# Kernel tuning notes

Hardware: AMD Instinct MI355X
Metric: run time of the kernel (lower is better)

Reference implementation:

```python
import jax, jax.numpy as jnp
import numpy as np

K = 3            # pairwise_size
DIL = 2          # pairwise_dilation
COLOR_THRESH = 0.3
EOS_COEF = 0.1


def unfold_wo_center(x, k, d):
    """x: [N,1,H,W] -> [N,1,k*k-1,H,W]; zero-padded dilated neighborhood, center removed
    (equivalent to F.unfold(x, k, padding=(k//2)*d, dilation=d) minus center tap)."""
    N, C, H, W = x.shape
    pad = (k // 2) * d
    xp = jnp.pad(x, ((0, 0), (0, 0), (pad, pad), (pad, pad)))
    c = k // 2
    patches = []
    for i in range(k):
        for j in range(k):
            if i == c and j == c:
                continue
            patches.append(xp[:, :, i * d:i * d + H, j * d:j * d + W])
    return jnp.stack(patches, axis=2)


def setup_inputs() -> dict:
    key = jax.random.key(0)
    k1, k2, k3, k4, k5 = jax.random.split(key, 5)
    B, Q, C1 = 2, 100, 81          # batch, queries, num_classes+1
    N, H, W = 64, 256, 256         # matched instances, mask resolution
    pred_logits = jax.random.normal(k1, (B, Q, C1), jnp.float32)
    target_classes = jax.random.randint(k2, (B, Q), 0, C1)
    src_masks = jax.random.normal(k3, (N, H, W), jnp.float32)
    target_box_masks = jax.random.randint(k4, (N, H, W), 0, 2).astype(jnp.int32)
    target_similarities = jax.random.uniform(k5, (N, K * K - 1, H, W), jnp.float32)
    empty_weight = jnp.ones((C1,), jnp.float32).at[-1].set(EOS_COEF)
    return {
        "pred_logits": pred_logits,
        "src_masks": src_masks,
        "empty_weight": empty_weight,
        "target_similarities": target_similarities,
        "target_classes": target_classes,
        "target_box_masks": target_box_masks,
        "num_masks": 64,
    }


def reference(pred_logits, src_masks, empty_weight, target_similarities,
              target_classes, target_box_masks, num_masks):
    nm = jnp.float32(max(int(num_masks), 1))

    # ---- loss_labels: weighted cross entropy (PyTorch weighted mean) ----
    logp = jax.nn.log_softmax(pred_logits.astype(jnp.float32), axis=-1)
    nll = -jnp.take_along_axis(logp, target_classes[..., None], axis=-1)[..., 0]
    w = empty_weight[target_classes]
    loss_ce = (w * nll).sum() / w.sum()

    # ---- loss_pairwise: BoxInst-style log-prob affinity over dilated neighborhood ----
    x = src_masks[:, None]                      # [N,1,H,W]
    lfg = jax.nn.log_sigmoid(x)
    lbg = jax.nn.log_sigmoid(-x)
    fg_u = unfold_wo_center(lfg, K, DIL)        # [N,1,8,H,W]
    bg_u = unfold_wo_center(lbg, K, DIL)
    a = lfg[:, :, None] + fg_u                  # log P(both fg)
    b = lbg[:, :, None] + bg_u                  # log P(both bg)
    m = jnp.maximum(a, b)
    log_same = jnp.log(jnp.exp(a - m) + jnp.exp(b - m)) + m
    sim = -log_same[:, 0]                       # [N,8,H,W]
    tgt = (target_similarities >= COLOR_THRESH).astype(jnp.float32) \
          * target_box_masks[:, None].astype(jnp.float32)
    loss_pairwise = (sim * tgt).sum() / jnp.maximum(tgt.sum(), 1.0) / nm
    # warmup_factor = 1.0 (iter >= pairwise_warmup_iters)

    # ---- loss_projection_masks: 1D projection dice ----
    eps = 0.001
    tb = target_box_masks.astype(jnp.float32)
    ix = jax.nn.sigmoid(src_masks.max(axis=2))  # project over W -> [N,H]
    iy = jax.nn.sigmoid(src_masks.max(axis=1))  # project over H -> [N,W]
    tx = tb.max(axis=2)
    ty = tb.max(axis=1)
    lx = 1.0 - 2.0 * (ix * tx).sum(1) / ((ix ** 2).sum(1) + (tx ** 2).sum(1) + eps)
    ly = 1.0 - 2.0 * (iy * ty).sum(1) / ((iy ** 2).sum(1) + (ty ** 2).sum(1) + eps)
    loss_proj = (lx + ly).sum() / nm

    return loss_ce + loss_pairwise + loss_proj
```

## Files before the change

kernel.cpp:

```cpp
#include <hip/hip_runtime.h>
#include <hip/hip_bf16.h>
#include <cmath>

#define H 256
#define W 256
#define NIMG 64
#define HW 65536
#define NBLK 2048
#define NWAVE (NBLK * 4)

typedef float vf4 __attribute__((ext_vector_type(4)));

__device__ inline float waveReduceSum(float v) {
#pragma unroll
    for (int o = 32; o > 0; o >>= 1) v += __shfl_xor(v, o, 64);
    return v;
}
__device__ inline float waveReduceMax(float v) {
#pragma unroll
    for (int o = 32; o > 0; o >>= 1) v = fmaxf(v, __shfl_xor(v, o, 64));
    return v;
}
__device__ inline float blockReduceSum(float v, float* s) {
    int lane = threadIdx.x & 63, wv = threadIdx.x >> 6;
    v = waveReduceSum(v);
    if (lane == 0) s[wv] = v;
    __syncthreads();
    float r = 0.f;
    if (wv == 0) {
        r = (lane < 4) ? s[lane] : 0.f;
        r = waveReduceSum(r);
    }
    __syncthreads();
    return r;
}

__global__ __launch_bounds__(256) void k_prep(
    const float* __restrict__ src, const int* __restrict__ bm,
    float* __restrict__ sigma,
    float* __restrict__ colpart_x, float* __restrict__ colpart_b,
    float* __restrict__ rowmax_x, float* __restrict__ rowmax_b)
{
    __shared__ float sx[32][4];
    __shared__ float sb[32][4];
    const int chunk = blockIdx.x, n = blockIdx.y, t = threadIdx.x;
    const int lane = t & 63, wv = t >> 6;
    const size_t base = (size_t)n * HW + chunk * 32 * W + t;
    const float* s = src + base;
    const int* b = bm + base;
    float* sg = sigma + base;
    float mx = -3.4e38f, mb = 0.f;
#pragma unroll 4
    for (int r = 0; r < 32; r++) {
        const float x = s[r * W];
        const float bf = (float)b[r * W];
        sg[r * W] = __builtin_amdgcn_rcpf(1.f + __expf(-x));
        mx = fmaxf(mx, x);
        mb = fmaxf(mb, bf);
        const float rx = waveReduceMax(x);
        const float rb = waveReduceMax(bf);
        if (lane == 0) { sx[r][wv] = rx; sb[r][wv] = rb; }
    }
    const int o = (n * 8 + chunk) * W + t;
    colpart_x[o] = mx;
    colpart_b[o] = mb;
    __syncthreads();
    if (t < 32) {
        rowmax_x[n * H + chunk * 32 + t] =
            fmaxf(fmaxf(sx[t][0], sx[t][1]), fmaxf(sx[t][2], sx[t][3]));
    } else if (t < 64) {
        const int r = t - 32;
        rowmax_b[n * H + chunk * 32 + r] =
            fmaxf(fmaxf(sb[r][0], sb[r][1]), fmaxf(sb[r][2], sb[r][3]));
    }
}

__global__ __launch_bounds__(256, 4) void k_stream(
    const float* __restrict__ ts, const int* __restrict__ bm,
    const float* __restrict__ sigma,
    float* __restrict__ part_st, float* __restrict__ part_t)
{
    const int t = threadIdx.x, lane = t & 63, wv = t >> 6;
    const int wid = blockIdx.x * 4 + wv;
    const int c0 = lane << 2;
    const int lm = (lane + 63) & 63, lp = (lane + 1) & 63;

    const int h  = wid & 255;
    const int p  = (wid >> 8) & 7;
    const int n0 = wid >> 11;

    const int DR = (p < 3) ? -2 : ((p < 5) ? 0 : 2);
    const int DC = (p == 0 || p == 3 || p == 5) ? -2 : ((p == 1 || p == 6) ? 0 : 2);
    const int hn = h + DR;
    const bool rv = (hn >= 0) && (hn < H);
    const int hnc = rv ? hn : h;

    const float* tsp0 = ts + ((size_t)(n0 * 8 + p)) * HW + (size_t)h * W + c0;
    const int*   bmp0 = bm + (size_t)n0 * HW + (size_t)h * W + c0;
    const float* scp0 = sigma + (size_t)n0 * HW + (size_t)h * W + c0;
    const float* snp0 = sigma + (size_t)n0 * HW + (size_t)hnc * W + c0;
    const size_t tstride = (size_t)4 * 8 * HW;
    const size_t istride = (size_t)4 * HW;

    float st = 0.f, tt = 0.f;

    vf4 Ats = __builtin_nontemporal_load(reinterpret_cast<const vf4*>(tsp0));
    int4   Abm = *reinterpret_cast<const int4*>(bmp0);
    float4 Asc = *reinterpret_cast<const float4*>(scp0);
    float4 Asn = *reinterpret_cast<const float4*>(snp0);

#pragma unroll 1
    for (int k = 0; k < 16; k++) {
        vf4 Bts = Ats; int4 Bbm = Abm; float4 Bsc = Asc; float4 Bsn = Asn;
        if (k < 15) {
            Bts = __builtin_nontemporal_load(
                reinterpret_cast<const vf4*>(tsp0 + (size_t)(k + 1) * tstride));
            Bbm = *reinterpret_cast<const int4*>(bmp0 + (size_t)(k + 1) * istride);
            Bsc = *reinterpret_cast<const float4*>(scp0 + (size_t)(k + 1) * istride);
            Bsn = *reinterpret_cast<const float4*>(snp0 + (size_t)(k + 1) * istride);
        }
        const float win[8] = {
            __shfl(Asn.z, lm, 64), __shfl(Asn.w, lm, 64),
            Asn.x, Asn.y, Asn.z, Asn.w,
            __shfl(Asn.x, lp, 64), __shfl(Asn.y, lp, 64)
        };
        const float scv[4] = {Asc.x, Asc.y, Asc.z, Asc.w};
        const float tsv[4] = {Ats.x, Ats.y, Ats.z, Ats.w};
        const int   bmv[4] = {Abm.x, Abm.y, Abm.z, Abm.w};
        float prod = 1.f;
#pragma unroll
        for (int i = 0; i < 4; i++) {
            const float sc = scv[i];
            const float bmf = (float)bmv[i];
            const bool thr = (tsv[i] >= 0.3f);
            tt += thr ? bmf : 0.f;
            const int col = c0 + i + DC;
            const bool valid = rv && (col >= 0) && (col < W);
            const float sn = (DC == -2) ? win[i] : ((DC == 0) ? win[i + 2] : win[i + 4]);
            const float P = fmaf(2.f * sc, sn, (1.f - sc) - sn);
            prod *= (thr && valid && (bmv[i] != 0)) ? P : 1.f;
        }
        st -= __logf(prod);
        Ats = Bts; Abm = Bbm; Asc = Bsc; Asn = Bsn;
    }
    const float wst = waveReduceSum(st);
    const float wtt = waveReduceSum(tt);
    if (lane == 0) { part_st[wid] = wst; part_t[wid] = wtt; }
}

__global__ __launch_bounds__(256) void k_proj(
    const float* __restrict__ colpart_x, const float* __restrict__ colpart_b,
    const float* __restrict__ rowmax_x, const float* __restrict__ rowmax_b,
    float* __restrict__ proj)
{
    __shared__ float red[4];
    const int n = blockIdx.x, t = threadIdx.x;
    float cx = -3.4e38f, cb = 0.f;
#pragma unroll
    for (int c = 0; c < 8; c++) {
        cx = fmaxf(cx, colpart_x[(n * 8 + c) * W + t]);
        cb = fmaxf(cb, colpart_b[(n * 8 + c) * W + t]);
    }
    const float iy = 1.f / (1.f + expf(-cx));
    const float ty = cb;
    const float ix = 1.f / (1.f + expf(-rowmax_x[n * H + t]));
    const float tx = rowmax_b[n * H + t];

    const float Sxy = blockReduceSum(ix * tx, red);
    const float Sxx = blockReduceSum(ix * ix, red);
    const float Stx = blockReduceSum(tx * tx, red);
    const float Syw = blockReduceSum(iy * ty, red);
    const float Syy = blockReduceSum(iy * iy, red);
    const float Sty = blockReduceSum(ty * ty, red);
    if (t == 0) {
        const float eps = 0.001f;
        const float lx = 1.f - 2.f * Sxy / (Sxx + Stx + eps);
        const float ly = 1.f - 2.f * Syw / (Syy + Sty + eps);
        proj[n] = lx + ly;
    }
}

__global__ __launch_bounds__(256) void k_final(
    const float* __restrict__ logits, const int* __restrict__ tcls,
    const float* __restrict__ ew, const int* __restrict__ num_masks,
    const float* __restrict__ part_st, const float* __restrict__ part_t,
    const float* __restrict__ proj, float* __restrict__ out)
{
    __shared__ float red[4];
    const int t = threadIdx.x;
    float s1 = 0.f, s2 = 0.f;
    for (int i = t; i < NWAVE; i += 256) { s1 += part_st[i]; s2 += part_t[i]; }
    const float sum_st = blockReduceSum(s1, red);
    const float sum_t = blockReduceSum(s2, red);
    const float pj = (t < NIMG) ? proj[t] : 0.f;
    const float sum_pj = blockReduceSum(pj, red);

    float wn = 0.f, wsum = 0.f;
    if (t < 200) {
        const float* row = logits + t * 81;
        float mx = -3.4e38f;
        for (int c = 0; c < 81; c++) mx = fmaxf(mx, row[c]);
        float se = 0.f;
        for (int c = 0; c < 81; c++) se += expf(row[c] - mx);
        const float lse = mx + logf(se);
        const int tc = tcls[t];
        const float nll = lse - row[tc];
        const float wv = ew[tc];
        wn = wv * nll;
        wsum = wv;
    }
    const float Swn = blockReduceSum(wn, red);
    const float Sw = blockReduceSum(wsum, red);
    if (t == 0) {
        const float nm = (float)max(num_masks[0], 1);
        const float loss_ce = Swn / Sw;
        const float loss_pw = sum_st / fmaxf(sum_t, 1.f) / nm;
        const float loss_pj = sum_pj / nm;
        out[0] = loss_ce + loss_pw + loss_pj;
    }
}

extern "C" void kernel_launch(void* const* d_in, const int* in_sizes, int n_in,
                              void* d_out, int out_size, void* d_ws, size_t ws_size,
                              hipStream_t stream) {
    const float* pred_logits = (const float*)d_in[0];
    const float* src         = (const float*)d_in[1];
    const float* ew          = (const float*)d_in[2];
    const float* ts          = (const float*)d_in[3];
    const int*   tcls        = (const int*)d_in[4];
    const int*   bm          = (const int*)d_in[5];
    const int*   nmasks      = (const int*)d_in[6];
    float* out = (float*)d_out;

    float* ws = (float*)d_ws;
    float* sigma     = ws;
    float* part_st   = ws + 4194304;
    float* part_t    = ws + 4202496;
    float* rowmax_x  = ws + 4210688;
    float* rowmax_b  = ws + 4227072;
    float* colpart_x = ws + 4243456;
    float* colpart_b = ws + 4374528;
    float* proj      = ws + 4505600;

    k_prep<<<dim3(8, NIMG), 256, 0, stream>>>(src, bm, sigma,
                                              colpart_x, colpart_b, rowmax_x, rowmax_b);
    k_stream<<<NBLK, 256, 0, stream>>>(ts, bm, sigma, part_st, part_t);
    k_proj<<<NIMG, 256, 0, stream>>>(colpart_x, colpart_b, rowmax_x, rowmax_b, proj);
    k_final<<<1, 256, 0, stream>>>(pred_logits, tcls, ew, nmasks, part_st, part_t, proj, out);
}
```

Measured before the change: 280.8 us.

## Move projection max reductions into stream kernel and remap waves to row strips

The prep kernel now only computes sigmoid with vectorized loads. The row and column max projections move into the stream kernel, computed on sigmoid values (sigmoid is monotonic) by the p==1 blocks. The stream kernel's work mapping changes so that each wave walks 16 consecutive rows of one image and one neighbor offset, instead of striding across images. This keeps the sigma and mask rows it shares with neighboring rows local. The aim is to cut redundant passes over src and the mask and to improve cache locality, at the cost of divergent extra work in one of the eight offset groups.

```diff
diff --git a/kernel.cpp b/kernel.cpp
--- a/kernel.cpp
+++ b/kernel.cpp
@@ -6,8 +6,9 @@
 #define W 256
 #define NIMG 64
 #define HW 65536
-#define NBLK 2048
-#define NWAVE (NBLK * 4)
+#define NSBLK 2048
+#define NWAVE (NSBLK * 4)
+#define NSTRIP 16
 
 typedef float vf4 __attribute__((ext_vector_type(4)));
 
@@ -36,94 +37,78 @@
 }
 
 __global__ __launch_bounds__(256) void k_prep(
-    const float* __restrict__ src, const int* __restrict__ bm,
-    float* __restrict__ sigma,
-    float* __restrict__ colpart_x, float* __restrict__ colpart_b,
-    float* __restrict__ rowmax_x, float* __restrict__ rowmax_b)
-{
-    __shared__ float sx[32][4];
-    __shared__ float sb[32][4];
-    const int chunk = blockIdx.x, n = blockIdx.y, t = threadIdx.x;
-    const int lane = t & 63, wv = t >> 6;
-    const size_t base = (size_t)n * HW + chunk * 32 * W + t;
-    const float* s = src + base;
-    const int* b = bm + base;
-    float* sg = sigma + base;
-    float mx = -3.4e38f, mb = 0.f;
-#pragma unroll 4
-    for (int r = 0; r < 32; r++) {
-        const float x = s[r * W];
-        const float bf = (float)b[r * W];
-        sg[r * W] = __builtin_amdgcn_rcpf(1.f + __expf(-x));
-        mx = fmaxf(mx, x);
-        mb = fmaxf(mb, bf);
-        const float rx = waveReduceMax(x);
-        const float rb = waveReduceMax(bf);
-        if (lane == 0) { sx[r][wv] = rx; sb[r][wv] = rb; }
-    }
-    const int o = (n * 8 + chunk) * W + t;
-    colpart_x[o] = mx;
-    colpart_b[o] = mb;
-    __syncthreads();
-    if (t < 32) {
-        rowmax_x[n * H + chunk * 32 + t] =
-            fmaxf(fmaxf(sx[t][0], sx[t][1]), fmaxf(sx[t][2], sx[t][3]));
-    } else if (t < 64) {
-        const int r = t - 32;
-        rowmax_b[n * H + chunk * 32 + r] =
-            fmaxf(fmaxf(sb[r][0], sb[r][1]), fmaxf(sb[r][2], sb[r][3]));
-    }
-}
-
-__global__ __launch_bounds__(256, 4) void k_stream(
+    const float* __restrict__ src, float* __restrict__ sigma)
+{
+    const vf4* s = reinterpret_cast<const vf4*>(src);
+    vf4* g = reinterpret_cast<vf4*>(sigma);
+    int i = blockIdx.x * 256 + threadIdx.x;
+#pragma unroll
+    for (int k = 0; k < 4; k++) {
+        vf4 x = s[i];
+        vf4 r;
+        r.x = __builtin_amdgcn_rcpf(1.f + __expf(-x.x));
+        r.y = __builtin_amdgcn_rcpf(1.f + __expf(-x.y));
+        r.z = __builtin_amdgcn_rcpf(1.f + __expf(-x.z));
+        r.w = __builtin_amdgcn_rcpf(1.f + __expf(-x.w));
+        g[i] = r;
+        i += 262144;
+    }
+}
+
+__global__ __launch_bounds__(256) void k_stream(
     const float* __restrict__ ts, const int* __restrict__ bm,
     const float* __restrict__ sigma,
-    float* __restrict__ part_st, float* __restrict__ part_t)
+    float* __restrict__ part_st, float* __restrict__ part_t,
+    float* __restrict__ rowsig, float* __restrict__ rowmax_b,
+    float* __restrict__ colpart_s, float* __restrict__ colpart_b)
 {
     const int t = threadIdx.x, lane = t & 63, wv = t >> 6;
-    const int wid = blockIdx.x * 4 + wv;
+    const int blk = blockIdx.x;
+    const int q = blk & 3, p = (blk >> 2) & 7, n = blk >> 5;
+    const int h0 = q * 64 + wv * 16;
     const int c0 = lane << 2;
     const int lm = (lane + 63) & 63, lp = (lane + 1) & 63;
-
-    const int h  = wid & 255;
-    const int p  = (wid >> 8) & 7;
-    const int n0 = wid >> 11;
-
     const int DR = (p < 3) ? -2 : ((p < 5) ? 0 : 2);
     const int DC = (p == 0 || p == 3 || p == 5) ? -2 : ((p == 1 || p == 6) ? 0 : 2);
-    const int hn = h + DR;
-    const bool rv = (hn >= 0) && (hn < H);
-    const int hnc = rv ? hn : h;
-
-    const float* tsp0 = ts + ((size_t)(n0 * 8 + p)) * HW + (size_t)h * W + c0;
-    const int*   bmp0 = bm + (size_t)n0 * HW + (size_t)h * W + c0;
-    const float* scp0 = sigma + (size_t)n0 * HW + (size_t)h * W + c0;
-    const float* snp0 = sigma + (size_t)n0 * HW + (size_t)hnc * W + c0;
-    const size_t tstride = (size_t)4 * 8 * HW;
-    const size_t istride = (size_t)4 * HW;
+
+    const float* tsp = ts + (size_t)(n * 8 + p) * HW;
+    const int*   bmn = bm + (size_t)n * HW;
+    const float* sgn = sigma + (size_t)n * HW;
 
     float st = 0.f, tt = 0.f;
-
-    vf4 Ats = __builtin_nontemporal_load(reinterpret_cast<const vf4*>(tsp0));
-    int4   Abm = *reinterpret_cast<const int4*>(bmp0);
-    float4 Asc = *reinterpret_cast<const float4*>(scp0);
-    float4 Asn = *reinterpret_cast<const float4*>(snp0);
-
+    float cms[4] = {0.f, 0.f, 0.f, 0.f};
+    float cmb[4] = {0.f, 0.f, 0.f, 0.f};
+
+    float4 Ats, Asc, Asn; int4 Abm;
+    {
+        const int h = h0, hnc = min(max(h + DR, 0), H - 1);
+        Ats = *reinterpret_cast<const float4*>(tsp + h * W + c0);
+        Abm = *reinterpret_cast<const int4*>(bmn + h * W + c0);
+        Asc = *reinterpret_cast<const float4*>(sgn + h * W + c0);
+        Asn = *reinterpret_cast<const float4*>(sgn + hnc * W + c0);
+    }
 #pragma unroll 1
-    for (int k = 0; k < 16; k++) {
-        vf4 Bts = Ats; int4 Bbm = Abm; float4 Bsc = Asc; float4 Bsn = Asn;
-        if (k < 15) {
-            Bts = __builtin_nontemporal_load(
-                reinterpret_cast<const vf4*>(tsp0 + (size_t)(k + 1) * tstride));
-            Bbm = *reinterpret_cast<const int4*>(bmp0 + (size_t)(k + 1) * istride);
-            Bsc = *reinterpret_cast<const float4*>(scp0 + (size_t)(k + 1) * istride);
-            Bsn = *reinterpret_cast<const float4*>(snp0 + (size_t)(k + 1) * istride);
-        }
-        const float win[8] = {
-            __shfl(Asn.z, lm, 64), __shfl(Asn.w, lm, 64),
-            Asn.x, Asn.y, Asn.z, Asn.w,
-            __shfl(Asn.x, lp, 64), __shfl(Asn.y, lp, 64)
-        };
+    for (int j = 0; j < 16; j++) {
+        const int h = h0 + j;
+        float4 Bts = Ats, Bsc = Asc, Bsn = Asn; int4 Bbm = Abm;
+        if (j < 15) {
+            const int h2 = h + 1, hnc2 = min(max(h2 + DR, 0), H - 1);
+            Bts = *reinterpret_cast<const float4*>(tsp + h2 * W + c0);
+            Bbm = *reinterpret_cast<const int4*>(bmn + h2 * W + c0);
+            Bsc = *reinterpret_cast<const float4*>(sgn + h2 * W + c0);
+            Bsn = *reinterpret_cast<const float4*>(sgn + hnc2 * W + c0);
+        }
+        const bool rv = (unsigned)(h + DR) < (unsigned)H;
+        float win[4];
+        if (DC == -2) {
+            win[0] = __shfl(Asn.z, lm, 64); win[1] = __shfl(Asn.w, lm, 64);
+            win[2] = Asn.x; win[3] = Asn.y;
+        } else if (DC == 0) {
+            win[0] = Asn.x; win[1] = Asn.y; win[2] = Asn.z; win[3] = Asn.w;
+        } else {
+            win[0] = Asn.z; win[1] = Asn.w;
+            win[2] = __shfl(Asn.x, lp, 64); win[3] = __shfl(Asn.y, lp, 64);
+        }
         const float scv[4] = {Asc.x, Asc.y, Asc.z, Asc.w};
         const float tsv[4] = {Ats.x, Ats.y, Ats.z, Ats.w};
         const int   bmv[4] = {Abm.x, Abm.y, Abm.z, Abm.w};
@@ -135,35 +120,49 @@
             const bool thr = (tsv[i] >= 0.3f);
             tt += thr ? bmf : 0.f;
             const int col = c0 + i + DC;
-            const bool valid = rv && (col >= 0) && (col < W);
-            const float sn = (DC == -2) ? win[i] : ((DC == 0) ? win[i + 2] : win[i + 4]);
-            const float P = fmaf(2.f * sc, sn, (1.f - sc) - sn);
+            const bool valid = rv && ((unsigned)col < (unsigned)W);
+            const float P = fmaf(2.f * sc, win[i], (1.f - sc) - win[i]);
             prod *= (thr && valid && (bmv[i] != 0)) ? P : 1.f;
+            if (p == 1) { cms[i] = fmaxf(cms[i], sc); cmb[i] = fmaxf(cmb[i], bmf); }
         }
         st -= __logf(prod);
+        if (p == 1) {
+            const float m4s = fmaxf(fmaxf(scv[0], scv[1]), fmaxf(scv[2], scv[3]));
+            const float m4b = fmaxf(fmaxf((float)bmv[0], (float)bmv[1]),
+                                    fmaxf((float)bmv[2], (float)bmv[3]));
+            const float wms = waveReduceMax(m4s);
+            const float wmb = waveReduceMax(m4b);
+            if (lane == 0) { rowsig[n * H + h] = wms; rowmax_b[n * H + h] = wmb; }
+        }
         Ats = Bts; Abm = Bbm; Asc = Bsc; Asn = Bsn;
+    }
+    if (p == 1) {
+        const int sidx = q * 4 + wv;
+        const int co = (n * NSTRIP + sidx) * W + c0;
+        *reinterpret_cast<float4*>(&colpart_s[co]) = make_float4(cms[0], cms[1], cms[2], cms[3]);
+        *reinterpret_cast<float4*>(&colpart_b[co]) = make_float4(cmb[0], cmb[1], cmb[2], cmb[3]);
     }
     const float wst = waveReduceSum(st);
     const float wtt = waveReduceSum(tt);
-    if (lane == 0) { part_st[wid] = wst; part_t[wid] = wtt; }
+    if (lane == 0) { const int wid = blk * 4 + wv; part_st[wid] = wst; part_t[wid] = wtt; }
 }
 
 __global__ __launch_bounds__(256) void k_proj(
-    const float* __restrict__ colpart_x, const float* __restrict__ colpart_b,
-    const float* __restrict__ rowmax_x, const float* __restrict__ rowmax_b,
+    const float* __restrict__ colpart_s, const float* __restrict__ colpart_b,
+    const float* __restrict__ rowsig, const float* __restrict__ rowmax_b,
     float* __restrict__ proj)
 {
     __shared__ float red[4];
     const int n = blockIdx.x, t = threadIdx.x;
-    float cx = -3.4e38f, cb = 0.f;
-#pragma unroll
-    for (int c = 0; c < 8; c++) {
-        cx = fmaxf(cx, colpart_x[(n * 8 + c) * W + t]);
-        cb = fmaxf(cb, colpart_b[(n * 8 + c) * W + t]);
-    }
-    const float iy = 1.f / (1.f + expf(-cx));
+    float cs = 0.f, cb = 0.f;
+#pragma unroll
+    for (int c = 0; c < NSTRIP; c++) {
+        cs = fmaxf(cs, colpart_s[(n * NSTRIP + c) * W + t]);
+        cb = fmaxf(cb, colpart_b[(n * NSTRIP + c) * W + t]);
+    }
+    const float iy = cs;
     const float ty = cb;
-    const float ix = 1.f / (1.f + expf(-rowmax_x[n * H + t]));
+    const float ix = rowsig[n * H + t];
     const float tx = rowmax_b[n * H + t];
 
     const float Sxy = blockReduceSum(ix * tx, red);
@@ -236,15 +235,15 @@
     float* sigma     = ws;
     float* part_st   = ws + 4194304;
     float* part_t    = ws + 4202496;
-    float* rowmax_x  = ws + 4210688;
+    float* rowsig    = ws + 4210688;
     float* rowmax_b  = ws + 4227072;
-    float* colpart_x = ws + 4243456;
-    float* colpart_b = ws + 4374528;
-    float* proj      = ws + 4505600;
-
-    k_prep<<<dim3(8, NIMG), 256, 0, stream>>>(src, bm, sigma,
-                                              colpart_x, colpart_b, rowmax_x, rowmax_b);
-    k_stream<<<NBLK, 256, 0, stream>>>(ts, bm, sigma, part_st, part_t);
-    k_proj<<<NIMG, 256, 0, stream>>>(colpart_x, colpart_b, rowmax_x, rowmax_b, proj);
+    float* colpart_s = ws + 4243456;
+    float* colpart_b = ws + 4505600;
+    float* proj      = ws + 4767744;
+
+    k_prep<<<1024, 256, 0, stream>>>(src, sigma);
+    k_stream<<<NSBLK, 256, 0, stream>>>(ts, bm, sigma, part_st, part_t,
+                                        rowsig, rowmax_b, colpart_s, colpart_b);
+    k_proj<<<NIMG, 256, 0, stream>>>(colpart_s, colpart_b, rowsig, rowmax_b, proj);
     k_final<<<1, 256, 0, stream>>>(pred_logits, tcls, ew, nmasks, part_st, part_t, proj, out);
 }
```

Measured after the change: 277.8 us. No clear change (-1.1%).
